# Optimization experiments

Measured on AMD Instinct MI355X. Metric: run time of the kernel, lower is better.

The kernel has to match this reference:

```python
import math
import jax, jax.numpy as jnp
import numpy as np

C = 1.0          # Poincare ball curvature
NUM_HEADS = 8
EPS = 1e-15

def _beta(a, b):
    # Beta function via lgamma (python float constant)
    return math.exp(math.lgamma(a) + math.lgamma(b) - math.lgamma(a + b))

def h_linear(x, z, r, c=C):
    """HNN++ Poincare fully-connected layer (hypll HLinear).
    x: [..., in] points in the ball; z: [in, out] tangent weights; r: [out] bias."""
    sc = math.sqrt(c)
    x2 = jnp.sum(x * x, axis=-1, keepdims=True)
    lam = 2.0 / (1.0 - c * x2)                                # conformal factor
    zn = jnp.maximum(jnp.linalg.norm(z, axis=0), EPS)          # [out]
    inner = x @ z                                              # [..., out]
    two_scr = 2.0 * sc * r
    d = (2.0 * zn / sc) * jnp.arcsinh(
        (sc * inner * lam / zn) * jnp.cosh(two_scr) - (lam - 1.0) * jnp.sinh(two_scr)
    )
    w = jnp.sinh(sc * d) / sc
    return w / (1.0 + jnp.sqrt(1.0 + c * jnp.sum(w * w, axis=-1, keepdims=True)))

def pairwise_dist(q, k, c=C):
    """Poincare distance d(q,k) = arccosh(1 + 2c|q-k|^2 / ((1-c|q|^2)(1-c|k|^2))) / sqrt(c).
    q,k: [B,H,S,hd] -> [B,H,S,S]."""
    q2 = jnp.sum(q * q, axis=-1)
    k2 = jnp.sum(k * k, axis=-1)
    qk = jnp.einsum('bhqd,bhkd->bhqk', q, k)
    diff2 = jnp.maximum(q2[..., :, None] + k2[..., None, :] - 2.0 * qk, 0.0)
    denom = (1.0 - c * q2)[..., :, None] * (1.0 - c * k2)[..., None, :]
    arg = 1.0 + 2.0 * c * diff2 / denom
    return jnp.arccosh(jnp.maximum(arg, 1.0 + 1e-7)) / math.sqrt(c)

def midpoint(v, w, c=C):
    """Weighted Mobius gyromidpoint: m = 1/2 (x) (sum w*lam*x / sum w*(lam-1)).
    v: [B,H,Sk,hd], w: [B,H,Sq,Sk] -> [B,H,Sq,hd]."""
    v2 = jnp.sum(v * v, axis=-1)                      # [B,H,Sk]
    lam = 2.0 / (1.0 - c * v2)
    num = jnp.einsum('bhqk,bhkd->bhqd', w * lam[..., None, :], v)
    den = jnp.maximum(jnp.einsum('bhqk,bhk->bhq', w, lam - 1.0), EPS)[..., None]
    g = num / den                                     # gyromidpoint pre-scaling
    sc = math.sqrt(c)
    gn = jnp.maximum(jnp.linalg.norm(g, axis=-1, keepdims=True), EPS)
    t = jnp.tanh(0.5 * jnp.arctanh(jnp.clip(sc * gn, 0.0, 1.0 - 1e-7)))
    return (t / sc) * g / gn

def _forward(query, key, value, Wq, bq, Wk, bk, Wv, bv, scale_tau, scale_gamma):
    B, S, E = query.shape
    H = NUM_HEADS
    hd = E // H
    # hyperbolic q/k/v projections, then split into heads: [B,H,S,hd]
    q = h_linear(query, Wq, bq).reshape(B, S, H, hd).transpose(0, 2, 1, 3)
    k = h_linear(key, Wk, bk).reshape(B, S, H, hd).transpose(0, 2, 1, 3)
    v = h_linear(value, Wv, bv).reshape(B, S, H, hd).transpose(0, 2, 1, 3)
    # similarity = -dist/tau - gamma with tau = exp(-scale_tau)
    sim = -pairwise_dist(q, k) * jnp.exp(scale_tau[0]) - scale_gamma[0]
    causal = jnp.triu(jnp.ones((S, S), dtype=bool), k=1)
    sim = jnp.where(causal, -jnp.inf, sim)
    w = jnp.exp(sim)                                  # 'exp' attention activation
    agg = midpoint(v, w)                              # [B,H,S,hd]
    agg = agg.transpose(0, 2, 1, 3).reshape(B, S, E)
    # HNN++ beta-concatenation of the per-head ball points
    scale = _beta(E / 2.0, 0.5) / _beta(hd / 2.0, 0.5)
    return agg * scale

def setup_inputs() -> dict:
    root = jax.random.key(0)
    ks = jax.random.split(root, 8)
    B, S, E = 1, 2048, 512
    s = 0.02  # keep points well inside the unit ball
    return {
        'query': s * jax.random.normal(ks[0], (B, S, E), jnp.float32),
        'key':   s * jax.random.normal(ks[1], (B, S, E), jnp.float32),
        'value': s * jax.random.normal(ks[2], (B, S, E), jnp.float32),
        'Wq': s * jax.random.normal(ks[3], (E, E), jnp.float32),
        'Wk': s * jax.random.normal(ks[4], (E, E), jnp.float32),
        'Wv': s * jax.random.normal(ks[5], (E, E), jnp.float32),
        'bq': jnp.zeros((E,), jnp.float32),
        'bk': jnp.zeros((E,), jnp.float32),
        'bv': jnp.zeros((E,), jnp.float32),
        'scale_tau': jnp.zeros((1,), jnp.float32),
        'scale_gamma': jnp.zeros((1,), jnp.float32),
    }

def reference(query, key, value, Wq, Wk, Wv, bq, bk, bv, scale_tau, scale_gamma):
    return _forward(query, key, value, Wq, bq, Wk, bk, Wv, bv, scale_tau, scale_gamma)
```

## Files before the change

### kernel.cpp

```cpp
#include <hip/hip_runtime.h>
#include <cmath>

#define H 8
#define SEQ 2048
#define EDIM 512
#define HD 64
#define EPSF 1e-15f

typedef short bf16x8 __attribute__((ext_vector_type(8)));
typedef float f32x4 __attribute__((ext_vector_type(4)));

#define FLAG_OFF  0
#define ZN_OFF    16
#define X2S_OFF   (ZN_OFF + 3 * EDIM)
#define STATS_OFF (X2S_OFF + 3 * SEQ)
#define U16_OFF   (STATS_OFF + 3 * H * SEQ + 16)
#define WT_U16    0
#define XB_U16    (WT_U16 + 3 * EDIM * EDIM)
#define QKVB_U16  (XB_U16 + 3 * SEQ * EDIM)
#define VT_U16    (QKVB_U16 + 3 * SEQ * EDIM)

__device__ __forceinline__ float bf2f(unsigned short u){
  union { unsigned int i; float f; } v; v.i = ((unsigned int)u) << 16; return v.f;
}
__device__ __forceinline__ unsigned short f2bf(float f){
  union { float f; unsigned int i; } v; v.f = f;
  unsigned int x = v.i;
  unsigned int r = (x + 0x7fffu + ((x >> 16) & 1u)) >> 16;
  return (unsigned short)r;
}

__global__ void probe_kernel(const unsigned short* __restrict__ q, int* __restrict__ flag){
  const int t = threadIdx.x;
  float mx = 0.f;
  #pragma unroll
  for (int j = 0; j < 4; ++j) mx = fmaxf(mx, fabsf(bf2f(q[t * 4 + j])));
  #pragma unroll
  for (int m = 32; m >= 1; m >>= 1) mx = fmaxf(mx, __shfl_xor(mx, m, 64));
  if (t == 0) *flag = (mx > 1000.f) ? 1 : 0;
}

__global__ __launch_bounds__(256) void wcvt_kernel(
    const void* __restrict__ Wq, const void* __restrict__ Wk, const void* __restrict__ Wv,
    const int* __restrict__ flag, unsigned short* __restrict__ WT, float* __restrict__ zn)
{
  const int p = blockIdx.y;
  const int bi = blockIdx.x >> 3, bo = blockIdx.x & 7;
  const void* W = (p == 0) ? Wq : ((p == 1) ? Wk : Wv);
  const int t = threadIdx.x;
  const int isf32 = *flag;
  __shared__ float tile[64][65];

  #pragma unroll
  for (int j = 0; j < 16; ++j){
    int idx = t + 256 * j;
    int il = idx >> 6, ol = idx & 63;
    float val;
    if (isf32) val = ((const float*)W)[(size_t)(bi * 64 + il) * EDIM + bo * 64 + ol];
    else       val = bf2f(((const unsigned short*)W)[(size_t)(bi * 64 + il) * EDIM + bo * 64 + ol]);
    tile[il][ol] = val;
  }
  __syncthreads();
  if (t < 64){
    float s = 0.f;
    #pragma unroll 8
    for (int i = 0; i < 64; ++i){ float v = tile[i][t]; s += v * v; }
    atomicAdd(&zn[p * EDIM + bo * 64 + t], s);
  }
  #pragma unroll
  for (int j = 0; j < 16; ++j){
    int idx = t + 256 * j;
    int ol = idx >> 6, il = idx & 63;
    WT[((size_t)p * EDIM + bo * 64 + ol) * EDIM + bi * 64 + il] = f2bf(tile[il][ol]);
  }
}

__global__ __launch_bounds__(256) void xcvt_kernel(
    const void* __restrict__ Xq, const void* __restrict__ Xk, const void* __restrict__ Xv,
    const int* __restrict__ flag, unsigned short* __restrict__ Xb, float* __restrict__ x2s)
{
  const int p = blockIdx.y;
  const void* X = (p == 0) ? Xq : ((p == 1) ? Xk : Xv);
  const int row = blockIdx.x * 8 + (threadIdx.x >> 5);
  const int l = threadIdx.x & 31;
  const int isf32 = *flag;
  float s = 0.f;
  #pragma unroll
  for (int j = 0; j < 16; ++j){
    int i = l + 32 * j;
    float val;
    if (isf32) val = ((const float*)X)[(size_t)row * EDIM + i];
    else       val = bf2f(((const unsigned short*)X)[(size_t)row * EDIM + i]);
    Xb[((size_t)p * SEQ + row) * EDIM + i] = f2bf(val);
    s += val * val;
  }
  #pragma unroll
  for (int m = 16; m >= 1; m >>= 1) s += __shfl_xor(s, m, 64);
  if (l == 0) x2s[p * SEQ + row] = s;
}

__global__ __launch_bounds__(256) void hlinear_kernel(
    const unsigned short* __restrict__ Xb, const unsigned short* __restrict__ WT,
    const void* __restrict__ Bq, const void* __restrict__ Bk, const void* __restrict__ Bv,
    const float* __restrict__ znacc, const float* __restrict__ x2s_g,
    const int* __restrict__ flag,
    unsigned short* __restrict__ qkvb, float* __restrict__ stats,
    unsigned short* __restrict__ VT)
{
  const int p = blockIdx.y;
  const void* Bb = (p == 0) ? Bq : ((p == 1) ? Bk : Bv);
  const int r0 = blockIdx.x * 8;
  const int t  = threadIdx.x;
  const int w = t >> 6, lane = t & 63;
  const int col = lane & 15, quad = lane >> 4;
  const int isf32 = *flag;

  __shared__ float smem[8 * EDIM];
  __shared__ float sw2[8];

  const unsigned short* Xrow = Xb + ((size_t)p * SEQ + r0 + (col & 7)) * EDIM;
  const unsigned short* WTb  = WT + ((size_t)p * EDIM + w * 128 + col) * EDIM;

  f32x4 acc[8];
  #pragma unroll
  for (int nt = 0; nt < 8; ++nt) acc[nt] = (f32x4){0.f, 0.f, 0.f, 0.f};

  for (int ks = 0; ks < 16; ++ks){
    bf16x8 af = *(const bf16x8*)&Xrow[ks * 32 + quad * 8];
    #pragma unroll
    for (int nt = 0; nt < 8; ++nt){
      bf16x8 bf = *(const bf16x8*)&WTb[(size_t)nt * 16 * EDIM + ks * 32 + quad * 8];
      acc[nt] = __builtin_amdgcn_mfma_f32_16x16x32_bf16(af, bf, acc[nt], 0, 0, 0);
    }
  }

  if (quad < 2){
    float lamr[4], lm1[4];
    #pragma unroll
    for (int r = 0; r < 4; ++r){
      float x2 = x2s_g[p * SEQ + r0 + quad * 4 + r];
      lamr[r] = 2.f / (1.f - x2);
      lm1[r] = lamr[r] - 1.f;
    }
    #pragma unroll
    for (int nt = 0; nt < 8; ++nt){
      const int n = w * 128 + nt * 16 + col;
      float znv = fmaxf(sqrtf(znacc[p * EDIM + n]), EPSF);
      float rb;
      if (isf32) rb = ((const float*)Bb)[n];
      else       rb = bf2f(((const unsigned short*)Bb)[n]);
      float e2r = __expf(2.f * rb);
      float ie2r = 1.f / e2r;
      float ch = 0.5f * (e2r + ie2r), sh = 0.5f * (e2r - ie2r);
      float izn = 1.f / znv;
      float tz = 2.f * znv;
      #pragma unroll
      for (int r = 0; r < 4; ++r){
        float a = (acc[nt][r] * lamr[r] * izn) * ch - lm1[r] * sh;
        float b = a + sqrtf(a * a + 1.f);
        float tt = __expf(tz * __logf(b));
        smem[(quad * 4 + r) * EDIM + n] = 0.5f * (tt - 1.f / tt);
      }
    }
  }
  __syncthreads();

  {
    int row = t >> 5, l = t & 31;
    float s = 0.f;
    for (int o = l; o < EDIM; o += 32){ float wv = smem[row * EDIM + o]; s += wv * wv; }
    #pragma unroll
    for (int m = 16; m >= 1; m >>= 1) s += __shfl_xor(s, m, 64);
    if (l == 0) sw2[row] = s;
  }
  __syncthreads();

  const int o0 = 2 * t;
  const int h0 = t >> 5;
  const int d0 = o0 & 63;
  #pragma unroll
  for (int rr = 0; rr < 8; ++rr){
    float inv = 1.f / (1.f + sqrtf(1.f + sw2[rr]));
    unsigned short b0 = f2bf(smem[rr * EDIM + o0] * inv);
    unsigned short b1 = f2bf(smem[rr * EDIM + o0 + 1] * inv);
    float r0v = bf2f(b0), r1v = bf2f(b1);
    int s = r0 + rr;
    unsigned int* dst = (unsigned int*)&qkvb[(((size_t)p * H + h0) * SEQ + s) * HD + d0];
    *dst = (unsigned int)b0 | ((unsigned int)b1 << 16);
    float ss = r0v * r0v + r1v * r1v;
    #pragma unroll
    for (int m = 16; m >= 1; m >>= 1) ss += __shfl_xor(ss, m, 64);
    if (p == 2){
      float lam = 2.f / (1.f - ss);
      VT[((size_t)h0 * 80 + d0) * SEQ + s]     = f2bf(r0v * lam);
      VT[((size_t)h0 * 80 + d0 + 1) * SEQ + s] = f2bf(r1v * lam);
      if ((t & 31) == 0) VT[((size_t)h0 * 80 + 64) * SEQ + s] = f2bf(lam - 1.f);
    }
    if ((t & 31) == 0) stats[((size_t)p * H + h0) * SEQ + s] = ss;
  }
}

__global__ __launch_bounds__(256) void attn_mfma_kernel(
    const unsigned short* __restrict__ Qb, const unsigned short* __restrict__ Kb,
    const unsigned short* __restrict__ VT,
    const float* __restrict__ q2s_all, const float* __restrict__ k2s_all,
    const void* __restrict__ tau, const void* __restrict__ gam,
    const int* __restrict__ flag,
    float* __restrict__ out, float beta_scale)
{
  const int h  = blockIdx.y;
  const int tile = blockIdx.x;
  const int t = threadIdx.x;
  const int w = t >> 6, lane = t & 63;
  const int col = lane & 15, quad = lane >> 4;
  const int q0 = tile * 16;

  const unsigned short* Qh  = Qb + (size_t)h * SEQ * HD;
  const unsigned short* Kh  = Kb + (size_t)h * SEQ * HD;
  const unsigned short* VTh = VT + (size_t)h * 80 * SEQ;
  const float* q2s = q2s_all + (size_t)h * SEQ;
  const float* k2s = k2s_all + (size_t)h * SEQ;

  __shared__ float red[4][64][20];

  float tauv, gamv;
  if (*flag){ tauv = ((const float*)tau)[0]; gamv = ((const float*)gam)[0]; }
  else      { tauv = bf2f(((const unsigned short*)tau)[0]);
              gamv = bf2f(((const unsigned short*)gam)[0]); }
  const float e_tau = expf(tauv);

  const int srcA = ((quad & 1) * 2) * 16 + col;
  const int srcB = srcA + 16;
  const int tsel = quad >> 1;

  bf16x8 qf0 = *(const bf16x8*)&Qh[(size_t)(q0 + col) * HD + quad * 8];
  bf16x8 qf1 = *(const bf16x8*)&Qh[(size_t)(q0 + col) * HD + 32 + quad * 8];
  const float q2 = q2s[q0 + col];
  const float omq2 = 1.f - q2;
  const int qmax = q0 + col;

  f32x4 pv[5];
  #pragma unroll
  for (int nt = 0; nt < 5; ++nt) pv[nt] = (f32x4){0.f, 0.f, 0.f, 0.f};

  const int nch = (tile + 4) >> 2;
  for (int kc = w; kc < nch; kc += 4){
    #pragma unroll
    for (int half = 0; half < 2; ++half){
      const int kb32 = kc * 64 + half * 32;
      unsigned int tlo[2], thi[2];
      #pragma unroll
      for (int tt = 0; tt < 2; ++tt){
        const int kbase = kb32 + 16 * tt;
        bf16x8 kf0 = *(const bf16x8*)&Kh[(size_t)(kbase + col) * HD + quad * 8];
        bf16x8 kf1 = *(const bf16x8*)&Kh[(size_t)(kbase + col) * HD + 32 + quad * 8];
        f32x4 s = (f32x4){0.f, 0.f, 0.f, 0.f};
        s = __builtin_amdgcn_mfma_f32_16x16x32_bf16(kf0, qf0, s, 0, 0, 0);
        s = __builtin_amdgcn_mfma_f32_16x16x32_bf16(kf1, qf1, s, 0, 0, 0);
        float4 k2q = *(const float4*)&k2s[kbase + quad * 4];
        unsigned short pb[4];
        #pragma unroll
        for (int r = 0; r < 4; ++r){
          float k2 = (r == 0) ? k2q.x : (r == 1) ? k2q.y : (r == 2) ? k2q.z : k2q.w;
          float diff2 = fmaxf(q2 + k2 - 2.f * s[r], 0.f);
          float u = 2.f * diff2 / (omq2 * (1.f - k2));
          u = fmaxf(u, 1e-7f);
          float z = 1.f + u + sqrtf(u * (u + 2.f));
          float dist = __logf(z);
          float wv = __expf(-e_tau * dist - gamv);
          int key = kbase + quad * 4 + r;
          if (key > qmax) wv = 0.f;
          pb[r] = f2bf(wv);
        }
        tlo[tt] = (unsigned int)pb[0] | ((unsigned int)pb[1] << 16);
        thi[tt] = (unsigned int)pb[2] | ((unsigned int)pb[3] << 16);
      }
      unsigned int a0 = (unsigned int)__shfl((int)tlo[0], srcA, 64);
      unsigned int a1 = (unsigned int)__shfl((int)tlo[1], srcA, 64);
      unsigned int b0 = (unsigned int)__shfl((int)thi[0], srcA, 64);
      unsigned int b1 = (unsigned int)__shfl((int)thi[1], srcA, 64);
      unsigned int c0 = (unsigned int)__shfl((int)tlo[0], srcB, 64);
      unsigned int c1 = (unsigned int)__shfl((int)tlo[1], srcB, 64);
      unsigned int d0 = (unsigned int)__shfl((int)thi[0], srcB, 64);
      unsigned int d1 = (unsigned int)__shfl((int)thi[1], srcB, 64);
      union { uint4 u; bf16x8 v; } pw;
      pw.u.x = tsel ? a1 : a0;
      pw.u.y = tsel ? b1 : b0;
      pw.u.z = tsel ? c1 : c0;
      pw.u.w = tsel ? d1 : d0;
      #pragma unroll
      for (int nt = 0; nt < 5; ++nt){
        bf16x8 vf = *(const bf16x8*)&VTh[(size_t)(16 * nt + col) * SEQ + kb32 + quad * 8];
        pv[nt] = __builtin_amdgcn_mfma_f32_16x16x32_bf16(pw.v, vf, pv[nt], 0, 0, 0);
      }
    }
  }

  #pragma unroll
  for (int nt = 0; nt < 5; ++nt)
    *(float4*)&red[w][lane][nt * 4] = (float4){pv[nt][0], pv[nt][1], pv[nt][2], pv[nt][3]};
  __syncthreads();

  if (t < 64){
    #pragma unroll
    for (int nt = 0; nt < 5; ++nt){
      float4 a = *(const float4*)&red[0][t][nt * 4];
      float4 b = *(const float4*)&red[1][t][nt * 4];
      float4 c = *(const float4*)&red[2][t][nt * 4];
      float4 d = *(const float4*)&red[3][t][nt * 4];
      pv[nt][0] = a.x + b.x + c.x + d.x;
      pv[nt][1] = a.y + b.y + c.y + d.y;
      pv[nt][2] = a.z + b.z + c.z + d.z;
      pv[nt][3] = a.w + b.w + c.w + d.w;
    }
    #pragma unroll
    for (int r = 0; r < 4; ++r){
      float den = __shfl(pv[4][r], quad * 16, 64);
      den = fmaxf(den, EPSF);
      float inv_den = 1.f / den;
      float g[4];
      float gsq = 0.f;
      #pragma unroll
      for (int nt = 0; nt < 4; ++nt){ g[nt] = pv[nt][r] * inv_den; gsq += g[nt] * g[nt]; }
      #pragma unroll
      for (int m = 8; m >= 1; m >>= 1) gsq += __shfl_xor(gsq, m, 64);
      float gn = fmaxf(sqrtf(gsq), EPSF);
      float x = fminf(gn, 1.f - 1e-7f);
      float tt2 = x / (1.f + sqrtf(1.f - x * x));
      float scl = (tt2 / gn) * beta_scale;
      const int q = q0 + quad * 4 + r;
      #pragma unroll
      for (int nt = 0; nt < 4; ++nt)
        out[(size_t)q * EDIM + h * HD + 16 * nt + col] = g[nt] * scl;
    }
  }
}

extern "C" void kernel_launch(void* const* d_in, const int* in_sizes, int n_in,
                              void* d_out, int out_size, void* d_ws, size_t ws_size,
                              hipStream_t stream){
  const void* Xq  = d_in[0];
  const void* Xk  = d_in[1];
  const void* Xv  = d_in[2];
  const void* Wq  = d_in[3];
  const void* Wk  = d_in[4];
  const void* Wv  = d_in[5];
  const void* Bq  = d_in[6];
  const void* Bk  = d_in[7];
  const void* Bv  = d_in[8];
  const void* tau = d_in[9];
  const void* gam = d_in[10];

  float* wsf   = (float*)d_ws;
  int*   flag  = (int*)(wsf + FLAG_OFF);
  float* zn    = wsf + ZN_OFF;
  float* x2s   = wsf + X2S_OFF;
  float* stats = wsf + STATS_OFF;
  unsigned short* u16b = (unsigned short*)(wsf + U16_OFF);
  unsigned short* WT   = u16b + WT_U16;
  unsigned short* Xb   = u16b + XB_U16;
  unsigned short* qkvb = u16b + QKVB_U16;
  unsigned short* VT   = u16b + VT_U16;

  unsigned short* Qb = qkvb;
  unsigned short* Kb = qkvb + (size_t)H * SEQ * HD;
  float* q2s = stats;
  float* k2s = stats + (size_t)H * SEQ;

  double lb1 = lgamma(EDIM / 2.0) + lgamma(0.5) - lgamma(EDIM / 2.0 + 0.5);
  double lb2 = lgamma(HD / 2.0)   + lgamma(0.5) - lgamma(HD / 2.0 + 0.5);
  float beta_scale = (float)exp(lb1 - lb2);

  probe_kernel<<<dim3(1), dim3(64), 0, stream>>>((const unsigned short*)Xq, flag);
  hipMemsetAsync(zn, 0, 3 * EDIM * sizeof(float), stream);
  hipMemsetAsync(VT, 0, (size_t)H * 80 * SEQ * sizeof(unsigned short), stream);
  wcvt_kernel<<<dim3(64, 3), dim3(256), 0, stream>>>(Wq, Wk, Wv, flag, WT, zn);
  xcvt_kernel<<<dim3(SEQ / 8, 3), dim3(256), 0, stream>>>(Xq, Xk, Xv, flag, Xb, x2s);
  hlinear_kernel<<<dim3(SEQ / 8, 3), dim3(256), 0, stream>>>(
      Xb, WT, Bq, Bk, Bv, zn, x2s, flag, qkvb, stats, VT);
  attn_mfma_kernel<<<dim3(SEQ / 16, H), dim3(256), 0, stream>>>(
      Qb, Kb, VT, q2s, k2s, tau, gam, flag, (float*)d_out, beta_scale);
}
```

Measured before the change: 231.3 us.

## Split attention key range across two blocks and precompute per-row reciprocal factors

```diff
diff --git a/kernel.cpp b/kernel.cpp
--- a/kernel.cpp
+++ b/kernel.cpp
@@ -14,11 +14,15 @@
 #define ZN_OFF    16
 #define X2S_OFF   (ZN_OFF + 3 * EDIM)
 #define STATS_OFF (X2S_OFF + 3 * SEQ)
-#define U16_OFF   (STATS_OFF + 3 * H * SEQ + 16)
+#define CQ_OFF    (STATS_OFF + 3 * H * SEQ)
+#define IK_OFF    (CQ_OFF + H * SEQ)
+#define U16_OFF   (IK_OFF + H * SEQ + 16)
 #define WT_U16    0
 #define XB_U16    (WT_U16 + 3 * EDIM * EDIM)
 #define QKVB_U16  (XB_U16 + 3 * SEQ * EDIM)
 #define VT_U16    (QKVB_U16 + 3 * SEQ * EDIM)
+#define U16_TOTAL (VT_U16 + H * 80 * SEQ)
+#define PART_OFF  (U16_OFF + (U16_TOTAL + 1) / 2 + 16)
 
 __device__ __forceinline__ float bf2f(unsigned short u){
   union { unsigned int i; float f; } v; v.i = ((unsigned int)u) << 16; return v.f;
@@ -105,6 +109,7 @@
     const float* __restrict__ znacc, const float* __restrict__ x2s_g,
     const int* __restrict__ flag,
     unsigned short* __restrict__ qkvb, float* __restrict__ stats,
+    float* __restrict__ cqs, float* __restrict__ iks,
     unsigned short* __restrict__ VT)
 {
   const int p = blockIdx.y;
@@ -196,20 +201,25 @@
       VT[((size_t)h0 * 80 + d0 + 1) * SEQ + s] = f2bf(r1v * lam);
       if ((t & 31) == 0) VT[((size_t)h0 * 80 + 64) * SEQ + s] = f2bf(lam - 1.f);
     }
-    if ((t & 31) == 0) stats[((size_t)p * H + h0) * SEQ + s] = ss;
-  }
-}
-
-__global__ __launch_bounds__(256) void attn_mfma_kernel(
+    if ((t & 31) == 0){
+      stats[((size_t)p * H + h0) * SEQ + s] = ss;
+      if (p == 0) cqs[(size_t)h0 * SEQ + s] = 2.f / (1.f - ss);
+      if (p == 1) iks[(size_t)h0 * SEQ + s] = 1.f / (1.f - ss);
+    }
+  }
+}
+
+__global__ __launch_bounds__(256) void attn_part_kernel(
     const unsigned short* __restrict__ Qb, const unsigned short* __restrict__ Kb,
     const unsigned short* __restrict__ VT,
     const float* __restrict__ q2s_all, const float* __restrict__ k2s_all,
+    const float* __restrict__ cqs_all, const float* __restrict__ iks_all,
     const void* __restrict__ tau, const void* __restrict__ gam,
-    const int* __restrict__ flag,
-    float* __restrict__ out, float beta_scale)
+    const int* __restrict__ flag, float4* __restrict__ part)
 {
   const int h  = blockIdx.y;
-  const int tile = blockIdx.x;
+  const int tile = blockIdx.x >> 1;
+  const int sl = blockIdx.x & 1;
   const int t = threadIdx.x;
   const int w = t >> 6, lane = t & 63;
   const int col = lane & 15, quad = lane >> 4;
@@ -220,6 +230,8 @@
   const unsigned short* VTh = VT + (size_t)h * 80 * SEQ;
   const float* q2s = q2s_all + (size_t)h * SEQ;
   const float* k2s = k2s_all + (size_t)h * SEQ;
+  const float* cqs = cqs_all + (size_t)h * SEQ;
+  const float* iks = iks_all + (size_t)h * SEQ;
 
   __shared__ float red[4][64][20];
 
@@ -236,7 +248,7 @@
   bf16x8 qf0 = *(const bf16x8*)&Qh[(size_t)(q0 + col) * HD + quad * 8];
   bf16x8 qf1 = *(const bf16x8*)&Qh[(size_t)(q0 + col) * HD + 32 + quad * 8];
   const float q2 = q2s[q0 + col];
-  const float omq2 = 1.f - q2;
+  const float cq = cqs[q0 + col];
   const int qmax = q0 + col;
 
   f32x4 pv[5];
@@ -244,7 +256,7 @@
   for (int nt = 0; nt < 5; ++nt) pv[nt] = (f32x4){0.f, 0.f, 0.f, 0.f};
 
   const int nch = (tile + 4) >> 2;
-  for (int kc = w; kc < nch; kc += 4){
+  for (int kc = sl * 4 + w; kc < nch; kc += 8){
     #pragma unroll
     for (int half = 0; half < 2; ++half){
       const int kb32 = kc * 64 + half * 32;
@@ -258,16 +270,17 @@
         s = __builtin_amdgcn_mfma_f32_16x16x32_bf16(kf0, qf0, s, 0, 0, 0);
         s = __builtin_amdgcn_mfma_f32_16x16x32_bf16(kf1, qf1, s, 0, 0, 0);
         float4 k2q = *(const float4*)&k2s[kbase + quad * 4];
+        float4 ikq = *(const float4*)&iks[kbase + quad * 4];
         unsigned short pb[4];
         #pragma unroll
         for (int r = 0; r < 4; ++r){
           float k2 = (r == 0) ? k2q.x : (r == 1) ? k2q.y : (r == 2) ? k2q.z : k2q.w;
+          float ik = (r == 0) ? ikq.x : (r == 1) ? ikq.y : (r == 2) ? ikq.z : ikq.w;
           float diff2 = fmaxf(q2 + k2 - 2.f * s[r], 0.f);
-          float u = 2.f * diff2 / (omq2 * (1.f - k2));
+          float u = diff2 * cq * ik;
           u = fmaxf(u, 1e-7f);
           float z = 1.f + u + sqrtf(u * (u + 2.f));
-          float dist = __logf(z);
-          float wv = __expf(-e_tau * dist - gamv);
+          float wv = __expf(-e_tau * __logf(z) - gamv);
           int key = kbase + quad * 4 + r;
           if (key > qmax) wv = 0.f;
           pb[r] = f2bf(wv);
@@ -302,37 +315,57 @@
   __syncthreads();
 
   if (t < 64){
+    const size_t base = (((size_t)h * 128 + tile) * 2 + sl) * 5;
     #pragma unroll
     for (int nt = 0; nt < 5; ++nt){
       float4 a = *(const float4*)&red[0][t][nt * 4];
       float4 b = *(const float4*)&red[1][t][nt * 4];
       float4 c = *(const float4*)&red[2][t][nt * 4];
       float4 d = *(const float4*)&red[3][t][nt * 4];
-      pv[nt][0] = a.x + b.x + c.x + d.x;
-      pv[nt][1] = a.y + b.y + c.y + d.y;
-      pv[nt][2] = a.z + b.z + c.z + d.z;
-      pv[nt][3] = a.w + b.w + c.w + d.w;
-    }
-    #pragma unroll
-    for (int r = 0; r < 4; ++r){
-      float den = __shfl(pv[4][r], quad * 16, 64);
-      den = fmaxf(den, EPSF);
-      float inv_den = 1.f / den;
-      float g[4];
-      float gsq = 0.f;
-      #pragma unroll
-      for (int nt = 0; nt < 4; ++nt){ g[nt] = pv[nt][r] * inv_den; gsq += g[nt] * g[nt]; }
-      #pragma unroll
-      for (int m = 8; m >= 1; m >>= 1) gsq += __shfl_xor(gsq, m, 64);
-      float gn = fmaxf(sqrtf(gsq), EPSF);
-      float x = fminf(gn, 1.f - 1e-7f);
-      float tt2 = x / (1.f + sqrtf(1.f - x * x));
-      float scl = (tt2 / gn) * beta_scale;
-      const int q = q0 + quad * 4 + r;
-      #pragma unroll
-      for (int nt = 0; nt < 4; ++nt)
-        out[(size_t)q * EDIM + h * HD + 16 * nt + col] = g[nt] * scl;
-    }
+      part[(base + nt) * 64 + t] =
+          (float4){a.x + b.x + c.x + d.x, a.y + b.y + c.y + d.y,
+                   a.z + b.z + c.z + d.z, a.w + b.w + c.w + d.w};
+    }
+  }
+}
+
+__global__ __launch_bounds__(64) void attn_fin_kernel(
+    const float4* __restrict__ part, float* __restrict__ out, float beta_scale)
+{
+  const int h = blockIdx.y, tile = blockIdx.x;
+  const int t = threadIdx.x;
+  const int col = t & 15, quad = t >> 4;
+  const int q0 = tile * 16;
+
+  f32x4 pv[5];
+  const size_t b0 = (((size_t)h * 128 + tile) * 2 + 0) * 5;
+  const size_t b1 = (((size_t)h * 128 + tile) * 2 + 1) * 5;
+  #pragma unroll
+  for (int nt = 0; nt < 5; ++nt){
+    float4 a = part[(b0 + nt) * 64 + t];
+    float4 b = part[(b1 + nt) * 64 + t];
+    pv[nt] = (f32x4){a.x + b.x, a.y + b.y, a.z + b.z, a.w + b.w};
+  }
+
+  #pragma unroll
+  for (int r = 0; r < 4; ++r){
+    float den = __shfl(pv[4][r], quad * 16, 64);
+    den = fmaxf(den, EPSF);
+    float inv_den = 1.f / den;
+    float g[4];
+    float gsq = 0.f;
+    #pragma unroll
+    for (int nt = 0; nt < 4; ++nt){ g[nt] = pv[nt][r] * inv_den; gsq += g[nt] * g[nt]; }
+    #pragma unroll
+    for (int m = 8; m >= 1; m >>= 1) gsq += __shfl_xor(gsq, m, 64);
+    float gn = fmaxf(sqrtf(gsq), EPSF);
+    float x = fminf(gn, 1.f - 1e-7f);
+    float tt2 = x / (1.f + sqrtf(1.f - x * x));
+    float scl = (tt2 / gn) * beta_scale;
+    const int q = q0 + quad * 4 + r;
+    #pragma unroll
+    for (int nt = 0; nt < 4; ++nt)
+      out[(size_t)q * EDIM + h * HD + 16 * nt + col] = g[nt] * scl;
   }
 }
 
@@ -356,11 +389,14 @@
   float* zn    = wsf + ZN_OFF;
   float* x2s   = wsf + X2S_OFF;
   float* stats = wsf + STATS_OFF;
+  float* cqs   = wsf + CQ_OFF;
+  float* iks   = wsf + IK_OFF;
   unsigned short* u16b = (unsigned short*)(wsf + U16_OFF);
   unsigned short* WT   = u16b + WT_U16;
   unsigned short* Xb   = u16b + XB_U16;
   unsigned short* qkvb = u16b + QKVB_U16;
   unsigned short* VT   = u16b + VT_U16;
+  float4* part = (float4*)(wsf + PART_OFF);
 
   unsigned short* Qb = qkvb;
   unsigned short* Kb = qkvb + (size_t)H * SEQ * HD;
@@ -377,7 +413,9 @@
   wcvt_kernel<<<dim3(64, 3), dim3(256), 0, stream>>>(Wq, Wk, Wv, flag, WT, zn);
   xcvt_kernel<<<dim3(SEQ / 8, 3), dim3(256), 0, stream>>>(Xq, Xk, Xv, flag, Xb, x2s);
   hlinear_kernel<<<dim3(SEQ / 8, 3), dim3(256), 0, stream>>>(
-      Xb, WT, Bq, Bk, Bv, zn, x2s, flag, qkvb, stats, VT);
-  attn_mfma_kernel<<<dim3(SEQ / 16, H), dim3(256), 0, stream>>>(
-      Qb, Kb, VT, q2s, k2s, tau, gam, flag, (float*)d_out, beta_scale);
-}
+      Xb, WT, Bq, Bk, Bv, zn, x2s, flag, qkvb, stats, cqs, iks, VT);
+  attn_part_kernel<<<dim3(256, H), dim3(256), 0, stream>>>(
+      Qb, Kb, VT, q2s, k2s, cqs, iks, tau, gam, flag, part);
+  attn_fin_kernel<<<dim3(128, H), dim3(64), 0, stream>>>(
+      part, (float*)d_out, beta_scale);
+}
```

New measurement: 231.6 us. About the same (+0.1%).
